# Performance work log

Hardware: AMD Instinct MI355X
Metric: run time of the kernel (lower is better)

Reference implementation:

```python
import jax, jax.numpy as jnp
import numpy as np

B, C, H, W, K, O, KS = 32, 16, 256, 256, 4, 16, 3
C4 = C // 4


def setup_inputs() -> dict:
    key = jax.random.key(0)
    ks = jax.random.split(key, 6)
    return {
        "x": jax.random.normal(ks[0], (B, C, H, W), dtype=jnp.float32),
        "weight": jax.random.normal(ks[1], (K, O, C, KS, KS), dtype=jnp.float32),
        "attn_w1": jax.random.normal(ks[2], (C4, C), dtype=jnp.float32) * 0.1,
        "attn_b1": jnp.zeros((C4,), dtype=jnp.float32),
        "attn_w2": jax.random.normal(ks[3], (K, C4), dtype=jnp.float32) * 0.1,
        "attn_b2": jnp.zeros((K,), dtype=jnp.float32),
    }


def reference(x, weight, attn_w1, attn_b1, attn_w2, attn_b2):
    # Attention branch: global avg pool -> 1x1 conv -> relu -> 1x1 conv -> softmax over K
    pooled = x.mean(axis=(2, 3))                                  # (B, C)
    h = jax.nn.relu(pooled @ attn_w1.T + attn_b1)                 # (B, C//4)
    attn = jax.nn.softmax(h @ attn_w2.T + attn_b2, axis=1)        # (B, K)

    # Per-sample aggregated kernel: sum_k attn[b,k] * weight[k]
    agg_w = jnp.einsum('bk,koihw->boihw', attn, weight)           # (B, O, C, KS, KS)

    # Per-sample conv2d (equivalent to torch grouped conv with groups=B)
    pad = ((1, 1), (1, 1))
    def per_sample(xi, wi):
        # xi: (C, H, W), wi: (O, C, KS, KS)
        return jax.lax.conv_general_dilated(
            xi[None], wi, window_strides=(1, 1), padding=pad,
            dimension_numbers=('NCHW', 'OIHW', 'NCHW'))[0]
    return jax.vmap(per_sample)(x, agg_w)                         # (B, O, H, W)
```

## Files before the change

kernel.cpp:

```cpp
#include <hip/hip_runtime.h>

#define BD  32
#define CD  16
#define HD  256
#define WD  256
#define KD  4
#define OD  16
#define C4D 4

__device__ float g_pooled[BD * CD];
__device__ float g_agg[BD * CD * 9 * OD];

__global__ void pool_kernel(const float* __restrict__ x) {
    const int plane = blockIdx.x;
    const float4* xp4 = reinterpret_cast<const float4*>(x + (size_t)plane * (HD * WD));

    float s = 0.f;
    #pragma unroll 4
    for (int j = threadIdx.x; j < HD * WD / 4; j += 256) {
        float4 v = xp4[j];
        s += v.x + v.y + v.z + v.w;
    }

    __shared__ float red[256];
    red[threadIdx.x] = s;
    __syncthreads();
    for (int off = 128; off > 0; off >>= 1) {
        if (threadIdx.x < off) red[threadIdx.x] += red[threadIdx.x + off];
        __syncthreads();
    }
    if (threadIdx.x == 0) g_pooled[plane] = red[0];
}

__global__ void attn_agg_kernel(const float* __restrict__ w1, const float* __restrict__ b1,
                                const float* __restrict__ w2, const float* __restrict__ b2,
                                const float* __restrict__ weight) {
    const int b = blockIdx.x;

    float p[CD];
    #pragma unroll
    for (int c = 0; c < CD; ++c) p[c] = g_pooled[b * CD + c] * (1.f / (HD * WD));

    float h[C4D];
    #pragma unroll
    for (int j = 0; j < C4D; ++j) {
        float s = b1[j];
        #pragma unroll
        for (int c = 0; c < CD; ++c) s = fmaf(p[c], w1[j * CD + c], s);
        h[j] = fmaxf(s, 0.f);
    }

    float lg[KD];
    float mx = -1e30f;
    #pragma unroll
    for (int k = 0; k < KD; ++k) {
        float s = b2[k];
        #pragma unroll
        for (int j = 0; j < C4D; ++j) s = fmaf(h[j], w2[k * C4D + j], s);
        lg[k] = s;
        mx = fmaxf(mx, s);
    }
    float se = 0.f;
    #pragma unroll
    for (int k = 0; k < KD; ++k) { lg[k] = expf(lg[k] - mx); se += lg[k]; }
    const float inv = 1.f / se;

    for (int idx = threadIdx.x; idx < CD * 9 * OD; idx += 256) {
        const int o   = idx & 15;
        const int t   = idx >> 4;
        const int c   = t / 9;
        const int tap = t - c * 9;
        float s = 0.f;
        #pragma unroll
        for (int k = 0; k < KD; ++k)
            s = fmaf(lg[k] * inv, weight[((k * OD + o) * CD + c) * 9 + tap], s);
        g_agg[b * (CD * 9 * OD) + idx] = s;
    }
}

__global__ __launch_bounds__(256, 3)
void conv_kernel(const float* __restrict__ x, float* __restrict__ out) {
    const int strip = blockIdx.x;
    const int b     = blockIdx.y;
    const int ct    = threadIdx.x;
    const int r0    = strip * 4;

    __shared__ float xlds[4][6][264];
    __shared__ float wlds[CD * 9 * OD];

    {
        const float* wb = g_agg + b * (CD * 9 * OD);
        for (int i = threadIdx.x; i < CD * 9 * OD; i += 256) wlds[i] = wb[i];
    }
    if (threadIdx.x < 48) {
        const int ch  = threadIdx.x / 12;
        const int rem = threadIdx.x % 12;
        xlds[ch][rem >> 1][(rem & 1) ? 260 : 3] = 0.f;
    }

    float acc[4][OD];
    #pragma unroll
    for (int r = 0; r < 4; ++r)
        #pragma unroll
        for (int o = 0; o < OD; ++o) acc[r][o] = 0.f;

    #define STAGE(gg)                                                            \
        _Pragma("unroll")                                                        \
        for (int i = 0; i < 6; ++i) {                                            \
            const int idx    = threadIdx.x + i * 256;                            \
            const int rowIdx = idx >> 6;                              \
            const int j      = idx & 63;                                         \
            const int ch     = rowIdx / 6;                                       \
            const int rr     = rowIdx - ch * 6;                                  \
            const int row    = r0 - 1 + rr;                                      \
            float4 v = make_float4(0.f, 0.f, 0.f, 0.f);                          \
            if (row >= 0 && row < HD)                                            \
                v = *reinterpret_cast<const float4*>(                            \
                    x + (size_t)(b * CD + (gg) * 4 + ch) * (HD * WD)             \
                      + row * WD + 4 * j);                                       \
            *reinterpret_cast<float4*>(&xlds[ch][rr][4 + 4 * j]) = v;            \
        }

    STAGE(0)
    __syncthreads();

    #pragma unroll 1
    for (int g = 0; g < 4; ++g) {
        #pragma unroll 1
        for (int ch = 0; ch < 4; ++ch) {
            float xw[6][3];
            #pragma unroll
            for (int rr = 0; rr < 6; ++rr)
                #pragma unroll
                for (int kk = 0; kk < 3; ++kk)
                    xw[rr][kk] = xlds[ch][rr][ct + 3 + kk];

            const float4* wc4 = reinterpret_cast<const float4*>(&wlds[(g * 4 + ch) * 144]);
            #pragma unroll
            for (int ky = 0; ky < 3; ++ky)
                #pragma unroll
                for (int kx = 0; kx < 3; ++kx)
                    #pragma unroll
                    for (int o4 = 0; o4 < 4; ++o4) {
                        const float4 w4 = wc4[(ky * 3 + kx) * 4 + o4];
                        #pragma unroll
                        for (int r = 0; r < 4; ++r) {
                            const float xv = xw[r + ky][kx];
                            acc[r][4 * o4 + 0] = fmaf(w4.x, xv, acc[r][4 * o4 + 0]);
                            acc[r][4 * o4 + 1] = fmaf(w4.y, xv, acc[r][4 * o4 + 1]);
                            acc[r][4 * o4 + 2] = fmaf(w4.z, xv, acc[r][4 * o4 + 2]);
                            acc[r][4 * o4 + 3] = fmaf(w4.w, xv, acc[r][4 * o4 + 3]);
                        }
                    }
        }
        __syncthreads();
        if (g < 3) {
            STAGE(g + 1)
            __syncthreads();
        }
    }
    #undef STAGE

    #pragma unroll
    for (int o = 0; o < OD; ++o)
        #pragma unroll
        for (int r = 0; r < 4; ++r)
            out[(((size_t)b * OD + o) * HD + (r0 + r)) * WD + ct] = acc[r][o];
}

extern "C" void kernel_launch(void* const* d_in, const int* in_sizes, int n_in,
                              void* d_out, int out_size, void* d_ws, size_t ws_size,
                              hipStream_t stream) {
    (void)in_sizes; (void)n_in; (void)out_size; (void)d_ws; (void)ws_size;
    const float* x      = (const float*)d_in[0];
    const float* weight = (const float*)d_in[1];
    const float* w1     = (const float*)d_in[2];
    const float* b1     = (const float*)d_in[3];
    const float* w2     = (const float*)d_in[4];
    const float* b2     = (const float*)d_in[5];
    float* out = (float*)d_out;

    pool_kernel<<<512, 256, 0, stream>>>(x);
    attn_agg_kernel<<<32, 256, 0, stream>>>(w1, b1, w2, b2, weight);
    conv_kernel<<<dim3(64, 32), 256, 0, stream>>>(x, out);
}
```

Before: 336.7 us.

## Run per-sample 3x3 conv on MFMA with split-bf16 precision

Replaces the FP32 FMA direct convolution with a 16x16 spatial-tile implicit GEMM built on 16x16x32 bf16 MFMA. Three products (hi*hi, lo*hi, hi*lo) approximate FP32 accuracy. The attention kernel now pre-packs the aggregated weights into MFMA B-fragments as hi/lo bf16 pairs. Inputs are converted to hi/lo bf16 in LDS with an 18x18 halo. This cuts FP32 ALU cost, but adds scalar global loads with conversion, uncoalesced halo reads and some precision loss.

```diff
diff --git a/kernel.cpp b/kernel.cpp
--- a/kernel.cpp
+++ b/kernel.cpp
@@ -8,8 +8,21 @@
 #define OD  16
 #define C4D 4
 
-__device__ float g_pooled[BD * CD];
-__device__ float g_agg[BD * CD * 9 * OD];
+typedef __attribute__((ext_vector_type(8))) short short8v;
+typedef __attribute__((ext_vector_type(4))) float float4v;
+
+__device__ float          g_pooled[BD * CD];
+__device__ unsigned short g_wfrag[BD * 2 * 5 * 64 * 8];
+
+__device__ __forceinline__ unsigned short bf16_rne(float f) {
+    unsigned u = __builtin_bit_cast(unsigned, f);
+    u += 0x7FFFu + ((u >> 16) & 1u);
+    return (unsigned short)(u >> 16);
+}
+__device__ __forceinline__ float bf16_to_f(unsigned short h) {
+    unsigned u = ((unsigned)h) << 16;
+    return __builtin_bit_cast(float, u);
+}
 
 __global__ void pool_kernel(const float* __restrict__ x) {
     const int plane = blockIdx.x;
@@ -64,108 +77,109 @@
     #pragma unroll
     for (int k = 0; k < KD; ++k) { lg[k] = expf(lg[k] - mx); se += lg[k]; }
     const float inv = 1.f / se;
-
-    for (int idx = threadIdx.x; idx < CD * 9 * OD; idx += 256) {
-        const int o   = idx & 15;
-        const int t   = idx >> 4;
-        const int c   = t / 9;
-        const int tap = t - c * 9;
-        float s = 0.f;
-        #pragma unroll
-        for (int k = 0; k < KD; ++k)
-            s = fmaf(lg[k] * inv, weight[((k * OD + o) * CD + c) * 9 + tap], s);
-        g_agg[b * (CD * 9 * OD) + idx] = s;
+    float at[KD];
+    #pragma unroll
+    for (int k = 0; k < KD; ++k) at[k] = lg[k] * inv;
+
+    for (int e = threadIdx.x; e < 5120; e += 256) {
+        const int prod = e / 2560;
+        const int rem  = e % 2560;
+        const int s    = rem / 512;
+        const int lr   = rem % 512;
+        const int lane = lr >> 3;
+        const int i    = lr & 7;
+        const int o    = lane & 15;
+        const int kg   = lane >> 4;
+        const int kk   = kg * 8 + i;
+        const int tl   = kk >> 4;
+        const int c    = kk & 15;
+        const int tap  = 2 * s + tl;
+        float v = 0.f;
+        if (tap < 9) {
+            #pragma unroll
+            for (int k = 0; k < KD; ++k)
+                v = fmaf(at[k], weight[((k * OD + o) * CD + c) * 9 + tap], v);
+        }
+        const unsigned short hi = bf16_rne(v);
+        unsigned short val = hi;
+        if (prod == 1) val = bf16_rne(v - bf16_to_f(hi));
+        g_wfrag[b * 5120 + e] = val;
     }
 }
 
 __global__ __launch_bounds__(256, 3)
 void conv_kernel(const float* __restrict__ x, float* __restrict__ out) {
-    const int strip = blockIdx.x;
-    const int b     = blockIdx.y;
-    const int ct    = threadIdx.x;
-    const int r0    = strip * 4;
-
-    __shared__ float xlds[4][6][264];
-    __shared__ float wlds[CD * 9 * OD];
-
+    const int b  = blockIdx.y;
+    const int tx = blockIdx.x & 15;
+    const int ty = blockIdx.x >> 4;
+    const int x0 = tx * 16, y0 = ty * 16;
+
+    __shared__ unsigned short xs[18 * 18 * 40];
+
+    for (int e = threadIdx.x; e < 5184; e += 256) {
+        const int c   = e / 324;
+        const int rem = e % 324;
+        const int r   = rem / 18;
+        const int col = rem % 18;
+        const int gy  = y0 - 1 + r;
+        const int gx  = x0 - 1 + col;
+        float v = 0.f;
+        if (gy >= 0 && gy < HD && gx >= 0 && gx < WD)
+            v = x[((size_t)(b * CD + c) * HD + gy) * WD + gx];
+        const unsigned short hi = bf16_rne(v);
+        const unsigned short lo = bf16_rne(v - bf16_to_f(hi));
+        const int base = (r * 18 + col) * 40 + (c >> 3) * 8 + (c & 7);
+        xs[base]      = hi;
+        xs[base + 16] = lo;
+    }
+
+    const int lane = threadIdx.x & 63;
+    const int wv   = threadIdx.x >> 6;
+
+    short8v whi[5], wlo[5];
     {
-        const float* wb = g_agg + b * (CD * 9 * OD);
-        for (int i = threadIdx.x; i < CD * 9 * OD; i += 256) wlds[i] = wb[i];
-    }
-    if (threadIdx.x < 48) {
-        const int ch  = threadIdx.x / 12;
-        const int rem = threadIdx.x % 12;
-        xlds[ch][rem >> 1][(rem & 1) ? 260 : 3] = 0.f;
-    }
-
-    float acc[4][OD];
-    #pragma unroll
-    for (int r = 0; r < 4; ++r)
-        #pragma unroll
-        for (int o = 0; o < OD; ++o) acc[r][o] = 0.f;
-
-    #define STAGE(gg)                                                            \
-        _Pragma("unroll")                                                        \
-        for (int i = 0; i < 6; ++i) {                                            \
-            const int idx    = threadIdx.x + i * 256;                            \
-            const int rowIdx = idx >> 6;                              \
-            const int j      = idx & 63;                                         \
-            const int ch     = rowIdx / 6;                                       \
-            const int rr     = rowIdx - ch * 6;                                  \
-            const int row    = r0 - 1 + rr;                                      \
-            float4 v = make_float4(0.f, 0.f, 0.f, 0.f);                          \
-            if (row >= 0 && row < HD)                                            \
-                v = *reinterpret_cast<const float4*>(                            \
-                    x + (size_t)(b * CD + (gg) * 4 + ch) * (HD * WD)             \
-                      + row * WD + 4 * j);                                       \
-            *reinterpret_cast<float4*>(&xlds[ch][rr][4 + 4 * j]) = v;            \
+        const unsigned short* wf = g_wfrag + b * 5120;
+        #pragma unroll
+        for (int s = 0; s < 5; ++s) {
+            whi[s] = *(const short8v*)&wf[s * 512 + lane * 8];
+            wlo[s] = *(const short8v*)&wf[2560 + s * 512 + lane * 8];
         }
-
-    STAGE(0)
+    }
+
+    const int m     = lane & 15;
+    const int kg    = lane >> 4;
+    const int tl    = kg >> 1;
+    const int chalf = kg & 1;
+    int aoff[5];
+    #pragma unroll
+    for (int s = 0; s < 5; ++s) {
+        int tap = 2 * s + tl;
+        if (tap > 8) tap = 8;
+        const int dy = tap / 3 - 1, dx = tap % 3 - 1;
+        aoff[s] = (dy * 18 + dx) * 40;
+    }
+
     __syncthreads();
 
-    #pragma unroll 1
-    for (int g = 0; g < 4; ++g) {
-        #pragma unroll 1
-        for (int ch = 0; ch < 4; ++ch) {
-            float xw[6][3];
-            #pragma unroll
-            for (int rr = 0; rr < 6; ++rr)
-                #pragma unroll
-                for (int kk = 0; kk < 3; ++kk)
-                    xw[rr][kk] = xlds[ch][rr][ct + 3 + kk];
-
-            const float4* wc4 = reinterpret_cast<const float4*>(&wlds[(g * 4 + ch) * 144]);
-            #pragma unroll
-            for (int ky = 0; ky < 3; ++ky)
-                #pragma unroll
-                for (int kx = 0; kx < 3; ++kx)
-                    #pragma unroll
-                    for (int o4 = 0; o4 < 4; ++o4) {
-                        const float4 w4 = wc4[(ky * 3 + kx) * 4 + o4];
-                        #pragma unroll
-                        for (int r = 0; r < 4; ++r) {
-                            const float xv = xw[r + ky][kx];
-                            acc[r][4 * o4 + 0] = fmaf(w4.x, xv, acc[r][4 * o4 + 0]);
-                            acc[r][4 * o4 + 1] = fmaf(w4.y, xv, acc[r][4 * o4 + 1]);
-                            acc[r][4 * o4 + 2] = fmaf(w4.z, xv, acc[r][4 * o4 + 2]);
-                            acc[r][4 * o4 + 3] = fmaf(w4.w, xv, acc[r][4 * o4 + 3]);
-                        }
-                    }
+    #pragma unroll
+    for (int q = 0; q < 4; ++q) {
+        const int rl   = wv * 4 + q;
+        const int pix0 = ((rl + 1) * 18 + (1 + m)) * 40 + chalf * 8;
+        float4v acc = {0.f, 0.f, 0.f, 0.f};
+        #pragma unroll
+        for (int s = 0; s < 5; ++s) {
+            const short8v ahi = *(const short8v*)&xs[pix0 + aoff[s]];
+            const short8v alo = *(const short8v*)&xs[pix0 + aoff[s] + 16];
+            acc = __builtin_amdgcn_mfma_f32_16x16x32_bf16(ahi, whi[s], acc, 0, 0, 0);
+            acc = __builtin_amdgcn_mfma_f32_16x16x32_bf16(alo, whi[s], acc, 0, 0, 0);
+            acc = __builtin_amdgcn_mfma_f32_16x16x32_bf16(ahi, wlo[s], acc, 0, 0, 0);
         }
-        __syncthreads();
-        if (g < 3) {
-            STAGE(g + 1)
-            __syncthreads();
-        }
-    }
-    #undef STAGE
-
-    #pragma unroll
-    for (int o = 0; o < OD; ++o)
-        #pragma unroll
-        for (int r = 0; r < 4; ++r)
-            out[(((size_t)b * OD + o) * HD + (r0 + r)) * WD + ct] = acc[r][o];
+        const int o = lane & 15;
+        const int y = y0 + rl;
+        float4 v4 = make_float4(acc[0], acc[1], acc[2], acc[3]);
+        *reinterpret_cast<float4*>(
+            &out[((size_t)(b * OD + o) * HD + y) * WD + x0 + kg * 4]) = v4;
+    }
 }
 
 extern "C" void kernel_launch(void* const* d_in, const int* in_sizes, int n_in,
@@ -182,5 +196,5 @@
 
     pool_kernel<<<512, 256, 0, stream>>>(x);
     attn_agg_kernel<<<32, 256, 0, stream>>>(w1, b1, w2, b2, weight);
-    conv_kernel<<<dim3(64, 32), 256, 0, stream>>>(x, out);
-}
+    conv_kernel<<<dim3(256, 32), 256, 0, stream>>>(x, out);
+}
```

Result: faster. 325.4 us (-3.4%).
